# Performance work log

Hardware: AMD Instinct MI355X
Metric: run time of the kernel (lower is better)

Reference implementation:

```python
import jax, jax.numpy as jnp
import numpy as np

B, T, D, H = 2, 2048, 1024, 16
HS = D // H  # head_size = 64
EPS = 1e-5


def layer_norm(x, g, b):
    mu = jnp.mean(x, axis=-1, keepdims=True)
    var = jnp.var(x, axis=-1, keepdims=True)
    return (x - mu) * jax.lax.rsqrt(var + EPS) * g + b


def setup_inputs() -> dict:
    key = jax.random.key(0)
    ks = jax.random.split(key, 12)
    s_attn = 1.0 / np.sqrt(D)
    s_ff1 = 1.0 / np.sqrt(D)
    s_ff2 = 1.0 / np.sqrt(4 * D)
    return {
        "x": jax.random.normal(ks[0], (B, T, D), jnp.float32),
        "Wq": jax.random.normal(ks[1], (H, D, HS), jnp.float32) * s_attn,
        "Wk": jax.random.normal(ks[2], (H, D, HS), jnp.float32) * s_attn,
        "Wv": jax.random.normal(ks[3], (H, D, HS), jnp.float32) * s_attn,
        "Wo": jax.random.normal(ks[4], (H * HS, D), jnp.float32) * (1.0 / np.sqrt(H * HS)),
        "bo": jnp.zeros((D,), jnp.float32),
        "W1": jax.random.normal(ks[5], (D, 4 * D), jnp.float32) * s_ff1,
        "b1": jnp.zeros((4 * D,), jnp.float32),
        "W2": jax.random.normal(ks[6], (4 * D, D), jnp.float32) * s_ff2,
        "b2": jnp.zeros((D,), jnp.float32),
        "ln1_g": jnp.ones((D,), jnp.float32),
        "ln1_b": jnp.zeros((D,), jnp.float32),
        "ln2_g": jnp.ones((D,), jnp.float32),
        "ln2_b": jnp.zeros((D,), jnp.float32),
    }


def reference(x, Wq, Wk, Wv, Wo, bo, W1, b1, W2, b2, ln1_g, ln1_b, ln2_g, ln2_b):
    # --- self-attention on ln1(x) ---
    h = layer_norm(x, ln1_g, ln1_b)
    Q = jnp.einsum('bsd,hdk->bhsk', h, Wq)
    K = jnp.einsum('bsd,hdk->bhsk', h, Wk)
    V = jnp.einsum('bsd,hdk->bhsk', h, Wv)
    scores = jnp.einsum('bhqk,bhsk->bhqs', Q, K) * (HS ** -0.5)
    attn = jax.nn.softmax(scores, axis=-1)  # [B,H,T,T] non-causal, as in source
    out = jnp.einsum('bhqs,bhsk->bhqk', attn, V)
    out = out.transpose(0, 2, 1, 3).reshape(B, T, H * HS)  # concat heads
    sa = out @ Wo + bo
    x = x + sa
    # --- feed-forward on ln2(x) ---
    h2 = layer_norm(x, ln2_g, ln2_b)
    ff = jax.nn.relu(h2 @ W1 + b1) @ W2 + b2
    return x + ff
```

## Files before the change

kernel.cpp:

```cpp
#include <hip/hip_runtime.h>
#include <cstdint>
#include <cmath>

typedef __bf16 bf16;
typedef __bf16 bf16x8 __attribute__((ext_vector_type(8)));
typedef __bf16 bf16x4 __attribute__((ext_vector_type(4)));
typedef float  f32x4  __attribute__((ext_vector_type(4)));

#define B_   2
#define T_   2048
#define D_   1024
#define H_   16
#define HS_  64
#define NTOK (B_ * T_)

typedef __attribute__((address_space(1))) uint8_t* gp1_t;
typedef __attribute__((address_space(3))) uint8_t* lp3_t;
__device__ __forceinline__ void gl_lds16(const void* g, void* l) {
    __builtin_amdgcn_global_load_lds((gp1_t)(uintptr_t)g,
                                     (lp3_t)(uint32_t)(uintptr_t)l,
                                     16, 0, 0);
}

__device__ __forceinline__ f32x4 mfma16(bf16x8 a, bf16x8 b, f32x4 c) {
    return __builtin_amdgcn_mfma_f32_16x16x32_bf16(a, b, c, 0, 0, 0);
}

__global__ void tcast(const float* __restrict__ in, bf16* __restrict__ out,
                      int R, int C) {
    __shared__ float t[32][33];
    const int c0 = blockIdx.x * 32, r0 = blockIdx.y * 32;
    for (int i = 0; i < 4; i++) {
        int r = threadIdx.y + i * 8;
        t[r][threadIdx.x] = in[(size_t)(r0 + r) * C + c0 + threadIdx.x];
    }
    __syncthreads();
    for (int i = 0; i < 4; i++) {
        int rr = threadIdx.y + i * 8;
        out[(size_t)(c0 + rr) * R + r0 + threadIdx.x] = (bf16)t[threadIdx.x][rr];
    }
}

__global__ void qkv_pack(const float* __restrict__ Wq, const float* __restrict__ Wk,
                         const float* __restrict__ Wv, bf16* __restrict__ out) {
    const int z = blockIdx.z;
    const int qkv = z >> 4;
    const float* in = (qkv == 0 ? Wq : qkv == 1 ? Wk : Wv) + (size_t)(z & 15) * D_ * HS_;
    bf16* o = out + (size_t)z * HS_ * D_;
    __shared__ float t[32][33];
    const int c0 = blockIdx.x * 32, r0 = blockIdx.y * 32;
    for (int i = 0; i < 4; i++) {
        int r = threadIdx.y + i * 8;
        t[r][threadIdx.x] = in[(size_t)(r0 + r) * HS_ + c0 + threadIdx.x];
    }
    __syncthreads();
    for (int i = 0; i < 4; i++) {
        int rr = threadIdx.y + i * 8;
        o[(size_t)(c0 + rr) * D_ + r0 + threadIdx.x] = (bf16)t[threadIdx.x][rr];
    }
}

__global__ __launch_bounds__(256) void ln_kernel(const float* __restrict__ x,
                                                 const float* __restrict__ g,
                                                 const float* __restrict__ b,
                                                 bf16* __restrict__ out) {
    const int row = blockIdx.x;
    const int tid = threadIdx.x;
    const float4 v = ((const float4*)(x + (size_t)row * 1024))[tid];
    float s  = v.x + v.y + v.z + v.w;
    float s2 = v.x * v.x + v.y * v.y + v.z * v.z + v.w * v.w;
    for (int m = 1; m < 64; m <<= 1) {
        s  += __shfl_xor(s, m);
        s2 += __shfl_xor(s2, m);
    }
    __shared__ float rs[4], rq[4];
    const int lane = tid & 63, wv = tid >> 6;
    if (lane == 0) { rs[wv] = s; rq[wv] = s2; }
    __syncthreads();
    s  = rs[0] + rs[1] + rs[2] + rs[3];
    s2 = rq[0] + rq[1] + rq[2] + rq[3];
    const float mu   = s * (1.f / 1024.f);
    const float var  = s2 * (1.f / 1024.f) - mu * mu;
    const float rstd = rsqrtf(var + 1e-5f);
    const float4 gg = ((const float4*)g)[tid];
    const float4 bb = ((const float4*)b)[tid];
    bf16x4 o;
    o[0] = (bf16)((v.x - mu) * rstd * gg.x + bb.x);
    o[1] = (bf16)((v.y - mu) * rstd * gg.y + bb.y);
    o[2] = (bf16)((v.z - mu) * rstd * gg.z + bb.z);
    o[3] = (bf16)((v.w - mu) * rstd * gg.w + bb.w);
    *(bf16x4*)(out + (size_t)row * 1024 + tid * 4) = o;
}

__global__ __launch_bounds__(256) void combine2(const float* __restrict__ p0,
                                                const float* __restrict__ p1,
                                                const float* __restrict__ resid,
                                                const float* __restrict__ bias,
                                                float* __restrict__ out) {
    const int i4 = blockIdx.x * 256 + threadIdx.x;
    const float4 a = ((const float4*)p0)[i4];
    const float4 b = ((const float4*)p1)[i4];
    const float4 r = ((const float4*)resid)[i4];
    const float4 bb = ((const float4*)bias)[i4 & 255];
    float4 o;
    o.x = a.x + b.x + r.x + bb.x;
    o.y = a.y + b.y + r.y + bb.y;
    o.z = a.z + b.z + r.z + bb.z;
    o.w = a.w + b.w + r.w + bb.w;
    ((float4*)out)[i4] = o;
}

__global__ __launch_bounds__(256) void attn_combine(const bf16* __restrict__ Opart,
                                                    const float* __restrict__ lpart,
                                                    bf16* __restrict__ attn) {
    const int i4 = blockIdx.x * 256 + threadIdx.x;
    const int tok = i4 >> 8;
    const int c = (i4 & 255) * 4;
    const int h = c >> 6;
    const int b = tok >> 11, t = tok & 2047;
    const int bh = b * 16 + h;
    const float l = lpart[(size_t)bh * T_ + t] + lpart[(size_t)(32 + bh) * T_ + t];
    const float inv = 1.f / l;
    const bf16x4 o0 = *(const bf16x4*)&Opart[(size_t)i4 * 4];
    const bf16x4 o1 = *(const bf16x4*)&Opart[(size_t)NTOK * 1024 + (size_t)i4 * 4];
    bf16x4 o;
    o[0] = (bf16)(((float)o0[0] + (float)o1[0]) * inv);
    o[1] = (bf16)(((float)o0[1] + (float)o1[1]) * inv);
    o[2] = (bf16)(((float)o0[2] + (float)o1[2]) * inv);
    o[3] = (bf16)(((float)o0[3] + (float)o1[3]) * inv);
    *(bf16x4*)&attn[(size_t)tok * 1024 + c] = o;
}

template <int BIAS, int RELU, int RES, int OUTBF16, int VTP = 0>
__global__ __launch_bounds__(512, 4) void gemm_bt(
    const bf16* __restrict__ A, const bf16* __restrict__ Bt,
    const float* __restrict__ bias, const float* __restrict__ resid,
    void* __restrict__ Cout, bf16* __restrict__ Vt, int M, int N, int K) {
    __shared__ __align__(16) bf16 As[2][128 * 32];
    __shared__ __align__(16) bf16 Bs[2][128 * 32];
    const int tid  = threadIdx.x;
    const int lane = tid & 63, w = tid >> 6;
    const int quad = lane >> 4, l15 = lane & 15;
    const int m0 = blockIdx.y * 128, n0 = blockIdx.x * 128;
    const int wm = (w & 3) * 32, wn = (w >> 2) * 64;

    f32x4 acc[2][4];
    for (int i = 0; i < 2; i++)
        for (int j = 0; j < 4; j++) acc[i][j] = f32x4{0.f, 0.f, 0.f, 0.f};

    const int arow = lane >> 2;
    const int acol = (lane & 3) * 8;

    for (int kt = 0; kt < K; kt += 64) {
        gl_lds16(A  + (size_t)(m0 + w * 16 + arow) * K + kt + acol,      &As[0][w * 512]);
        gl_lds16(A  + (size_t)(m0 + w * 16 + arow) * K + kt + 32 + acol, &As[1][w * 512]);
        gl_lds16(Bt + (size_t)(n0 + w * 16 + arow) * K + kt + acol,      &Bs[0][w * 512]);
        gl_lds16(Bt + (size_t)(n0 + w * 16 + arow) * K + kt + 32 + acol, &Bs[1][w * 512]);
        __syncthreads();
        for (int kh = 0; kh < 2; kh++) {
            bf16x8 af[2], bfr[4];
            for (int mi = 0; mi < 2; mi++)
                af[mi] = *(const bf16x8*)&As[kh][(wm + mi * 16 + l15) * 32 + quad * 8];
            for (int ni = 0; ni < 4; ni++)
                bfr[ni] = *(const bf16x8*)&Bs[kh][(wn + ni * 16 + l15) * 32 + quad * 8];
            for (int mi = 0; mi < 2; mi++)
                for (int ni = 0; ni < 4; ni++)
                    acc[mi][ni] = mfma16(af[mi], bfr[ni], acc[mi][ni]);
        }
        __syncthreads();
    }

    for (int mi = 0; mi < 2; mi++) {
        for (int ni = 0; ni < 4; ni++) {
            const int colb = n0 + wn + ni * 16 + l15;
            if (VTP && colb >= 2048) {
                const int h = (colb - 2048) >> 6, hs = (colb - 2048) & 63;
                const int row0 = m0 + wm + mi * 16 + quad * 4;
                const int b = row0 >> 11;
                bf16x4 p4;
                p4[0] = (bf16)acc[mi][ni][0];
                p4[1] = (bf16)acc[mi][ni][1];
                p4[2] = (bf16)acc[mi][ni][2];
                p4[3] = (bf16)acc[mi][ni][3];
                *(bf16x4*)&Vt[((size_t)(b * 16 + h) * 64 + hs) * T_ + (row0 & 2047)] = p4;
                continue;
            }
            const float bv = BIAS ? bias[colb] : 0.f;
            for (int r = 0; r < 4; r++) {
                const int row = m0 + wm + mi * 16 + quad * 4 + r;
                float v = acc[mi][ni][r] + bv;
                if (RELU) v = fmaxf(v, 0.f);
                if (RES)  v += resid[(size_t)row * N + colb];
                if (OUTBF16) ((bf16*)Cout)[(size_t)row * N + colb] = (bf16)v;
                else         ((float*)Cout)[(size_t)row * N + colb] = v;
            }
        }
    }
}

__global__ __launch_bounds__(512, 4) void gemm_bt_partial(
    const bf16* __restrict__ A, const bf16* __restrict__ Bt,
    float* __restrict__ Cpart, int M, int N, int K) {
    __shared__ __align__(16) bf16 As[2][128 * 32];
    __shared__ __align__(16) bf16 Bs[2][128 * 32];
    const int tid  = threadIdx.x;
    const int lane = tid & 63, w = tid >> 6;
    const int quad = lane >> 4, l15 = lane & 15;
    const int m0 = blockIdx.y * 128, n0 = blockIdx.x * 128;
    const int wm = (w & 3) * 32, wn = (w >> 2) * 64;
    const int kpb = K / gridDim.z;
    const int k0 = blockIdx.z * kpb, k1 = k0 + kpb;
    float* Cz = Cpart + (size_t)blockIdx.z * M * N;

    f32x4 acc[2][4];
    for (int i = 0; i < 2; i++)
        for (int j = 0; j < 4; j++) acc[i][j] = f32x4{0.f, 0.f, 0.f, 0.f};

    const int arow = lane >> 2;
    const int acol = (lane & 3) * 8;

    for (int kt = k0; kt < k1; kt += 64) {
        gl_lds16(A  + (size_t)(m0 + w * 16 + arow) * K + kt + acol,      &As[0][w * 512]);
        gl_lds16(A  + (size_t)(m0 + w * 16 + arow) * K + kt + 32 + acol, &As[1][w * 512]);
        gl_lds16(Bt + (size_t)(n0 + w * 16 + arow) * K + kt + acol,      &Bs[0][w * 512]);
        gl_lds16(Bt + (size_t)(n0 + w * 16 + arow) * K + kt + 32 + acol, &Bs[1][w * 512]);
        __syncthreads();
        for (int kh = 0; kh < 2; kh++) {
            bf16x8 af[2], bfr[4];
            for (int mi = 0; mi < 2; mi++)
                af[mi] = *(const bf16x8*)&As[kh][(wm + mi * 16 + l15) * 32 + quad * 8];
            for (int ni = 0; ni < 4; ni++)
                bfr[ni] = *(const bf16x8*)&Bs[kh][(wn + ni * 16 + l15) * 32 + quad * 8];
            for (int mi = 0; mi < 2; mi++)
                for (int ni = 0; ni < 4; ni++)
                    acc[mi][ni] = mfma16(af[mi], bfr[ni], acc[mi][ni]);
        }
        __syncthreads();
    }

    for (int mi = 0; mi < 2; mi++) {
        for (int ni = 0; ni < 4; ni++) {
            const int colb = n0 + wn + ni * 16 + l15;
            for (int r = 0; r < 4; r++) {
                const int row = m0 + wm + mi * 16 + quad * 4 + r;
                Cz[(size_t)row * N + colb] = acc[mi][ni][r];
            }
        }
    }
}

#define LSTR 68
#define NJH  16
__global__ __launch_bounds__(256, 2) void flash_attn(const bf16* __restrict__ QKV,
                                                     const bf16* __restrict__ Vt,
                                                     bf16* __restrict__ Opart,
                                                     float* __restrict__ lpart) {
    const int bh = blockIdx.y, b = bh >> 4, h = bh & 15;
    const int q0 = blockIdx.x * 256;
    const int z = blockIdx.z;
    const int jbeg = z * NJH;
    const int tid = threadIdx.x, lane = tid & 63, w = tid >> 6;
    const int quad = lane >> 4, l15 = lane & 15;
    __shared__ __align__(16) bf16 Ks[64 * LSTR];
    __shared__ __align__(16) bf16 Vs[64 * LSTR];
    __shared__ __align__(16) bf16 Ps[256 * LSTR];
    const bf16* Qb = QKV + (size_t)b * T_ * 3072 + h * 64;
    const bf16* Kb = QKV + (size_t)b * T_ * 3072 + 1024 + h * 64;
    const bf16* Vb = Vt  + (size_t)bh * HS_ * T_;

    const float sc = 0.125f * 1.44269504088896f;
    const int sr = tid >> 2, scc = (tid & 3) * 16;

    bf16x8 QA[4][2];
    for (int qnt = 0; qnt < 4; qnt++) {
        const size_t row = (size_t)(q0 + w * 64 + qnt * 16 + l15) * 3072;
        for (int kk = 0; kk < 2; kk++) {
            bf16x8 q = *(const bf16x8*)&Qb[row + kk * 32 + quad * 8];
            for (int i = 0; i < 8; i++) q[i] = (bf16)((float)q[i] * sc);
            QA[qnt][kk] = q;
        }
    }

    bf16x8 ones8;
    for (int i = 0; i < 8; i++) ones8[i] = (bf16)1.0f;

    f32x4 O[4][4], lacc[4];
    for (int mi = 0; mi < 4; mi++) {
        lacc[mi] = f32x4{0.f, 0.f, 0.f, 0.f};
        for (int n = 0; n < 4; n++) O[mi][n] = f32x4{0.f, 0.f, 0.f, 0.f};
    }

    bf16x8 k0, k1, v0, v1;
    {
        const int s0 = jbeg * 64;
        k0 = *(const bf16x8*)&Kb[(size_t)(s0 + sr) * 3072 + scc];
        k1 = *(const bf16x8*)&Kb[(size_t)(s0 + sr) * 3072 + scc + 8];
        v0 = *(const bf16x8*)&Vb[(size_t)sr * T_ + s0 + scc];
        v1 = *(const bf16x8*)&Vb[(size_t)sr * T_ + s0 + scc + 8];
    }

    for (int jj = 0; jj < NJH; jj++) {
        __syncthreads();
        *(bf16x8*)&Ks[sr * LSTR + scc]     = k0;
        *(bf16x8*)&Ks[sr * LSTR + scc + 8] = k1;
        *(bf16x8*)&Vs[sr * LSTR + scc]     = v0;
        *(bf16x8*)&Vs[sr * LSTR + scc + 8] = v1;
        __syncthreads();
        if (jj + 1 < NJH) {
            const int s1 = (jbeg + jj + 1) * 64;
            k0 = *(const bf16x8*)&Kb[(size_t)(s1 + sr) * 3072 + scc];
            k1 = *(const bf16x8*)&Kb[(size_t)(s1 + sr) * 3072 + scc + 8];
            v0 = *(const bf16x8*)&Vb[(size_t)sr * T_ + s1 + scc];
            v1 = *(const bf16x8*)&Vb[(size_t)sr * T_ + s1 + scc + 8];
        }
        bf16x8 KB[4][2];
        for (int smt = 0; smt < 4; smt++)
            for (int kk = 0; kk < 2; kk++)
                KB[smt][kk] = *(const bf16x8*)&Ks[(smt * 16 + l15) * LSTR + kk * 32 + quad * 8];
        for (int qnt = 0; qnt < 4; qnt++) {
            f32x4 ST[4];
            for (int smt = 0; smt < 4; smt++) ST[smt] = f32x4{0.f, 0.f, 0.f, 0.f};
            for (int kk = 0; kk < 2; kk++)
                for (int smt = 0; smt < 4; smt++)
                    ST[smt] = mfma16(KB[smt][kk], QA[qnt][kk], ST[smt]);
            const int prow = (w * 64 + qnt * 16 + l15) * LSTR + quad * 4;
            for (int smt = 0; smt < 4; smt++) {
                bf16x4 p4;
                p4[0] = (bf16)__builtin_amdgcn_exp2f(ST[smt][0]);
                p4[1] = (bf16)__builtin_amdgcn_exp2f(ST[smt][1]);
                p4[2] = (bf16)__builtin_amdgcn_exp2f(ST[smt][2]);
                p4[3] = (bf16)__builtin_amdgcn_exp2f(ST[smt][3]);
                *(bf16x4*)&Ps[prow + smt * 16] = p4;
            }
        }
        bf16x8 VB[4][2];
        for (int n = 0; n < 4; n++)
            for (int kk = 0; kk < 2; kk++)
                VB[n][kk] = *(const bf16x8*)&Vs[(n * 16 + l15) * LSTR + kk * 32 + quad * 8];
        for (int mi = 0; mi < 4; mi++) {
            const int pr = (w * 64 + mi * 16 + l15) * LSTR + quad * 8;
            bf16x8 PA0 = *(const bf16x8*)&Ps[pr];
            bf16x8 PA1 = *(const bf16x8*)&Ps[pr + 32];
            for (int n = 0; n < 4; n++) {
                O[mi][n] = mfma16(PA0, VB[n][0], O[mi][n]);
                O[mi][n] = mfma16(PA1, VB[n][1], O[mi][n]);
            }
            lacc[mi] = mfma16(PA0, ones8, lacc[mi]);
            lacc[mi] = mfma16(PA1, ones8, lacc[mi]);
        }
    }

    bf16* Oz = Opart + (size_t)z * NTOK * 1024;
    for (int mi = 0; mi < 4; mi++) {
        for (int r = 0; r < 4; r++) {
            const size_t tok = (size_t)b * T_ + q0 + w * 64 + mi * 16 + quad * 4 + r;
            for (int n = 0; n < 4; n++)
                Oz[tok * 1024 + h * 64 + n * 16 + l15] = (bf16)O[mi][n][r];
        }
        if (l15 == 0)
            *(f32x4*)&lpart[((size_t)z * 32 + bh) * T_ + q0 + w * 64 + mi * 16 + quad * 4] = lacc[mi];
    }
}

extern "C" void kernel_launch(void* const* d_in, const int* in_sizes, int n_in,
                              void* d_out, int out_size, void* d_ws, size_t ws_size,
                              hipStream_t stream) {
    const float* x   = (const float*)d_in[0];
    const float* Wq  = (const float*)d_in[1];
    const float* Wk  = (const float*)d_in[2];
    const float* Wv  = (const float*)d_in[3];
    const float* Wo  = (const float*)d_in[4];
    const float* bo  = (const float*)d_in[5];
    const float* W1  = (const float*)d_in[6];
    const float* b1  = (const float*)d_in[7];
    const float* W2  = (const float*)d_in[8];
    const float* b2  = (const float*)d_in[9];
    const float* g1  = (const float*)d_in[10];
    const float* be1 = (const float*)d_in[11];
    const float* g2  = (const float*)d_in[12];
    const float* be2 = (const float*)d_in[13];

    char* ws = (char*)d_ws;
    const size_t MB = 1ull << 20;
    bf16*  WqkvT = (bf16*)(ws);
    bf16*  WoT   = (bf16*)(ws + 6  * MB);
    bf16*  W1T   = (bf16*)(ws + 8  * MB);
    bf16*  W2T   = (bf16*)(ws + 16 * MB);
    bf16*  hbuf  = (bf16*)(ws + 24 * MB);
    bf16*  QKV   = (bf16*)(ws + 32 * MB);
    bf16*  Vt    = (bf16*)(ws + 56 * MB);
    bf16*  attn  = (bf16*)(ws + 64 * MB);
    float* lpart = (float*)(ws + 72 * MB);
    float* x2    = (float*)(ws + 72 * MB);
    bf16*  ff1   = (bf16*)(ws + 32 * MB);
    bf16*  Opart = (bf16*)(ws + 88 * MB);
    float* part  = (float*)(ws + 88 * MB);
    float* out   = (float*)d_out;

    dim3 tb(32, 8);
    qkv_pack<<<dim3(2, 32, 48), tb, 0, stream>>>(Wq, Wk, Wv, WqkvT);
    tcast<<<dim3(32, 32),  tb, 0, stream>>>(Wo, WoT, 1024, 1024);
    tcast<<<dim3(128, 32), tb, 0, stream>>>(W1, W1T, 1024, 4096);
    tcast<<<dim3(32, 128), tb, 0, stream>>>(W2, W2T, 4096, 1024);
    ln_kernel<<<NTOK, 256, 0, stream>>>(x, g1, be1, hbuf);
    gemm_bt<0, 0, 0, 1, 1><<<dim3(24, 32), 512, 0, stream>>>(hbuf, WqkvT, nullptr, nullptr, QKV, Vt, NTOK, 3072, 1024);
    flash_attn<<<dim3(T_ / 256, B_ * H_, 2), 256, 0, stream>>>(QKV, Vt, Opart, lpart);
    attn_combine<<<NTOK, 256, 0, stream>>>(Opart, lpart, attn);
    gemm_bt<1, 0, 1, 0><<<dim3(8, 32), 512, 0, stream>>>(attn, WoT, bo, x, x2, nullptr, NTOK, 1024, 1024);
    ln_kernel<<<NTOK, 256, 0, stream>>>(x2, g2, be2, hbuf);
    gemm_bt<1, 1, 0, 1><<<dim3(32, 32), 512, 0, stream>>>(hbuf, W1T, b1, nullptr, ff1, nullptr, NTOK, 4096, 1024);
    gemm_bt_partial<<<dim3(8, 32, 2), 512, 0, stream>>>(ff1, W2T, part, NTOK, 1024, 4096);
    combine2<<<NTOK, 256, 0, stream>>>(part, part + (size_t)NTOK * 1024, x2, b2, out);
}
```

Measured before the change: 360.5 us.

## Use 4-warp 64x64-per-wave GEMM tiles and 4-way split-K for FF2

The QKV and FF1 GEMMs switch to 256-thread blocks in which each wave computes a 64x64 tile (4x4 MFMA fragments) instead of 32x64. This raises register-level reuse of the LDS fragments. The out-projection GEMM keeps the old 512-thread layout through a new gemm_bt512 copy. The FF2 GEMM now splits K four ways instead of two, and a combine4 kernel sums the four partials, trading more occupancy for extra partial-buffer traffic and workspace use.

```diff
diff --git a/kernel.cpp b/kernel.cpp
--- a/kernel.cpp
+++ b/kernel.cpp
@@ -92,21 +92,23 @@
     *(bf16x4*)(out + (size_t)row * 1024 + tid * 4) = o;
 }
 
-__global__ __launch_bounds__(256) void combine2(const float* __restrict__ p0,
-                                                const float* __restrict__ p1,
+__global__ __launch_bounds__(256) void combine4(const float* __restrict__ p,
                                                 const float* __restrict__ resid,
                                                 const float* __restrict__ bias,
                                                 float* __restrict__ out) {
     const int i4 = blockIdx.x * 256 + threadIdx.x;
-    const float4 a = ((const float4*)p0)[i4];
-    const float4 b = ((const float4*)p1)[i4];
+    const size_t stride4 = (size_t)NTOK * 256;
+    const float4 a = ((const float4*)p)[i4];
+    const float4 b = ((const float4*)p)[stride4 + i4];
+    const float4 c = ((const float4*)p)[2 * stride4 + i4];
+    const float4 d = ((const float4*)p)[3 * stride4 + i4];
     const float4 r = ((const float4*)resid)[i4];
     const float4 bb = ((const float4*)bias)[i4 & 255];
     float4 o;
-    o.x = a.x + b.x + r.x + bb.x;
-    o.y = a.y + b.y + r.y + bb.y;
-    o.z = a.z + b.z + r.z + bb.z;
-    o.w = a.w + b.w + r.w + bb.w;
+    o.x = a.x + b.x + c.x + d.x + r.x + bb.x;
+    o.y = a.y + b.y + c.y + d.y + r.y + bb.y;
+    o.z = a.z + b.z + c.z + d.z + r.z + bb.z;
+    o.w = a.w + b.w + c.w + d.w + r.w + bb.w;
     ((float4*)out)[i4] = o;
 }
 
@@ -132,7 +134,7 @@
 }
 
 template <int BIAS, int RELU, int RES, int OUTBF16, int VTP = 0>
-__global__ __launch_bounds__(512, 4) void gemm_bt(
+__global__ __launch_bounds__(256, 2) void gemm_bt(
     const bf16* __restrict__ A, const bf16* __restrict__ Bt,
     const float* __restrict__ bias, const float* __restrict__ resid,
     void* __restrict__ Cout, bf16* __restrict__ Vt, int M, int N, int K) {
@@ -142,35 +144,40 @@
     const int lane = tid & 63, w = tid >> 6;
     const int quad = lane >> 4, l15 = lane & 15;
     const int m0 = blockIdx.y * 128, n0 = blockIdx.x * 128;
-    const int wm = (w & 3) * 32, wn = (w >> 2) * 64;
-
-    f32x4 acc[2][4];
-    for (int i = 0; i < 2; i++)
+    const int wm = (w & 1) * 64, wn = (w >> 1) * 64;
+
+    f32x4 acc[4][4];
+    for (int i = 0; i < 4; i++)
         for (int j = 0; j < 4; j++) acc[i][j] = f32x4{0.f, 0.f, 0.f, 0.f};
 
     const int arow = lane >> 2;
     const int acol = (lane & 3) * 8;
+    const int c0 = w * 2, c1 = w * 2 + 1;
 
     for (int kt = 0; kt < K; kt += 64) {
-        gl_lds16(A  + (size_t)(m0 + w * 16 + arow) * K + kt + acol,      &As[0][w * 512]);
-        gl_lds16(A  + (size_t)(m0 + w * 16 + arow) * K + kt + 32 + acol, &As[1][w * 512]);
-        gl_lds16(Bt + (size_t)(n0 + w * 16 + arow) * K + kt + acol,      &Bs[0][w * 512]);
-        gl_lds16(Bt + (size_t)(n0 + w * 16 + arow) * K + kt + 32 + acol, &Bs[1][w * 512]);
+        gl_lds16(A  + (size_t)(m0 + c0 * 16 + arow) * K + kt + acol,      &As[0][c0 * 512]);
+        gl_lds16(A  + (size_t)(m0 + c1 * 16 + arow) * K + kt + acol,      &As[0][c1 * 512]);
+        gl_lds16(A  + (size_t)(m0 + c0 * 16 + arow) * K + kt + 32 + acol, &As[1][c0 * 512]);
+        gl_lds16(A  + (size_t)(m0 + c1 * 16 + arow) * K + kt + 32 + acol, &As[1][c1 * 512]);
+        gl_lds16(Bt + (size_t)(n0 + c0 * 16 + arow) * K + kt + acol,      &Bs[0][c0 * 512]);
+        gl_lds16(Bt + (size_t)(n0 + c1 * 16 + arow) * K + kt + acol,      &Bs[0][c1 * 512]);
+        gl_lds16(Bt + (size_t)(n0 + c0 * 16 + arow) * K + kt + 32 + acol, &Bs[1][c0 * 512]);
+        gl_lds16(Bt + (size_t)(n0 + c1 * 16 + arow) * K + kt + 32 + acol, &Bs[1][c1 * 512]);
         __syncthreads();
         for (int kh = 0; kh < 2; kh++) {
-            bf16x8 af[2], bfr[4];
-            for (int mi = 0; mi < 2; mi++)
+            bf16x8 af[4], bfr[4];
+            for (int mi = 0; mi < 4; mi++)
                 af[mi] = *(const bf16x8*)&As[kh][(wm + mi * 16 + l15) * 32 + quad * 8];
             for (int ni = 0; ni < 4; ni++)
                 bfr[ni] = *(const bf16x8*)&Bs[kh][(wn + ni * 16 + l15) * 32 + quad * 8];
-            for (int mi = 0; mi < 2; mi++)
+            for (int mi = 0; mi < 4; mi++)
                 for (int ni = 0; ni < 4; ni++)
                     acc[mi][ni] = mfma16(af[mi], bfr[ni], acc[mi][ni]);
         }
         __syncthreads();
     }
 
-    for (int mi = 0; mi < 2; mi++) {
+    for (int mi = 0; mi < 4; mi++) {
         for (int ni = 0; ni < 4; ni++) {
             const int colb = n0 + wn + ni * 16 + l15;
             if (VTP && colb >= 2048) {
@@ -185,6 +192,61 @@
                 *(bf16x4*)&Vt[((size_t)(b * 16 + h) * 64 + hs) * T_ + (row0 & 2047)] = p4;
                 continue;
             }
+            const float bv = BIAS ? bias[colb] : 0.f;
+            for (int r = 0; r < 4; r++) {
+                const int row = m0 + wm + mi * 16 + quad * 4 + r;
+                float v = acc[mi][ni][r] + bv;
+                if (RELU) v = fmaxf(v, 0.f);
+                if (RES)  v += resid[(size_t)row * N + colb];
+                if (OUTBF16) ((bf16*)Cout)[(size_t)row * N + colb] = (bf16)v;
+                else         ((float*)Cout)[(size_t)row * N + colb] = v;
+            }
+        }
+    }
+}
+
+template <int BIAS, int RELU, int RES, int OUTBF16>
+__global__ __launch_bounds__(512, 4) void gemm_bt512(
+    const bf16* __restrict__ A, const bf16* __restrict__ Bt,
+    const float* __restrict__ bias, const float* __restrict__ resid,
+    void* __restrict__ Cout, int M, int N, int K) {
+    __shared__ __align__(16) bf16 As[2][128 * 32];
+    __shared__ __align__(16) bf16 Bs[2][128 * 32];
+    const int tid  = threadIdx.x;
+    const int lane = tid & 63, w = tid >> 6;
+    const int quad = lane >> 4, l15 = lane & 15;
+    const int m0 = blockIdx.y * 128, n0 = blockIdx.x * 128;
+    const int wm = (w & 3) * 32, wn = (w >> 2) * 64;
+
+    f32x4 acc[2][4];
+    for (int i = 0; i < 2; i++)
+        for (int j = 0; j < 4; j++) acc[i][j] = f32x4{0.f, 0.f, 0.f, 0.f};
+
+    const int arow = lane >> 2;
+    const int acol = (lane & 3) * 8;
+
+    for (int kt = 0; kt < K; kt += 64) {
+        gl_lds16(A  + (size_t)(m0 + w * 16 + arow) * K + kt + acol,      &As[0][w * 512]);
+        gl_lds16(A  + (size_t)(m0 + w * 16 + arow) * K + kt + 32 + acol, &As[1][w * 512]);
+        gl_lds16(Bt + (size_t)(n0 + w * 16 + arow) * K + kt + acol,      &Bs[0][w * 512]);
+        gl_lds16(Bt + (size_t)(n0 + w * 16 + arow) * K + kt + 32 + acol, &Bs[1][w * 512]);
+        __syncthreads();
+        for (int kh = 0; kh < 2; kh++) {
+            bf16x8 af[2], bfr[4];
+            for (int mi = 0; mi < 2; mi++)
+                af[mi] = *(const bf16x8*)&As[kh][(wm + mi * 16 + l15) * 32 + quad * 8];
+            for (int ni = 0; ni < 4; ni++)
+                bfr[ni] = *(const bf16x8*)&Bs[kh][(wn + ni * 16 + l15) * 32 + quad * 8];
+            for (int mi = 0; mi < 2; mi++)
+                for (int ni = 0; ni < 4; ni++)
+                    acc[mi][ni] = mfma16(af[mi], bfr[ni], acc[mi][ni]);
+        }
+        __syncthreads();
+    }
+
+    for (int mi = 0; mi < 2; mi++) {
+        for (int ni = 0; ni < 4; ni++) {
+            const int colb = n0 + wn + ni * 16 + l15;
             const float bv = BIAS ? bias[colb] : 0.f;
             for (int r = 0; r < 4; r++) {
                 const int row = m0 + wm + mi * 16 + quad * 4 + r;
@@ -403,12 +465,12 @@
     tcast<<<dim3(128, 32), tb, 0, stream>>>(W1, W1T, 1024, 4096);
     tcast<<<dim3(32, 128), tb, 0, stream>>>(W2, W2T, 4096, 1024);
     ln_kernel<<<NTOK, 256, 0, stream>>>(x, g1, be1, hbuf);
-    gemm_bt<0, 0, 0, 1, 1><<<dim3(24, 32), 512, 0, stream>>>(hbuf, WqkvT, nullptr, nullptr, QKV, Vt, NTOK, 3072, 1024);
+    gemm_bt<0, 0, 0, 1, 1><<<dim3(24, 32), 256, 0, stream>>>(hbuf, WqkvT, nullptr, nullptr, QKV, Vt, NTOK, 3072, 1024);
     flash_attn<<<dim3(T_ / 256, B_ * H_, 2), 256, 0, stream>>>(QKV, Vt, Opart, lpart);
     attn_combine<<<NTOK, 256, 0, stream>>>(Opart, lpart, attn);
-    gemm_bt<1, 0, 1, 0><<<dim3(8, 32), 512, 0, stream>>>(attn, WoT, bo, x, x2, nullptr, NTOK, 1024, 1024);
+    gemm_bt512<1, 0, 1, 0><<<dim3(8, 32), 512, 0, stream>>>(attn, WoT, bo, x, x2, NTOK, 1024, 1024);
     ln_kernel<<<NTOK, 256, 0, stream>>>(x2, g2, be2, hbuf);
-    gemm_bt<1, 1, 0, 1><<<dim3(32, 32), 512, 0, stream>>>(hbuf, W1T, b1, nullptr, ff1, nullptr, NTOK, 4096, 1024);
-    gemm_bt_partial<<<dim3(8, 32, 2), 512, 0, stream>>>(ff1, W2T, part, NTOK, 1024, 4096);
-    combine2<<<NTOK, 256, 0, stream>>>(part, part + (size_t)NTOK * 1024, x2, b2, out);
-}
+    gemm_bt<1, 1, 0, 1><<<dim3(32, 32), 256, 0, stream>>>(hbuf, W1T, b1, nullptr, ff1, nullptr, NTOK, 4096, 1024);
+    gemm_bt_partial<<<dim3(8, 32, 4), 512, 0, stream>>>(ff1, W2T, part, NTOK, 1024, 4096);
+    combine4<<<NTOK, 256, 0, stream>>>(part, x2, b2, out);
+}
```

Result: slower. 370.5 us (+2.8%).
